# Kernel optimization log

Hardware: AMD Instinct MI355X
Metric: run time of the kernel (lower is better)

## Reference

```python
import jax, jax.numpy as jnp
import numpy as np

NUM_HIDDEN = 128
IN_DIM = 512  # num_hidden + num_in + num_vec*4 = 128 + 256 + 128
N_NODES = 50000
N_EDGES = 400000
BN_EPS = 1e-5


def setup_inputs() -> dict:
    key = jax.random.key(0)
    ks = jax.random.split(key, 12)
    h_V = jax.random.normal(ks[0], (N_NODES, NUM_HIDDEN), dtype=jnp.float32)
    h_E = jax.random.normal(ks[1], (N_EDGES, NUM_HIDDEN), dtype=jnp.float32)
    edge_idx = jax.random.randint(ks[2], (2, N_EDGES), 0, N_NODES, dtype=jnp.int64)
    batch_id = jnp.zeros((N_EDGES,), dtype=jnp.int32)
    vector_field_feat = jax.random.normal(ks[3], (N_EDGES, NUM_HIDDEN), dtype=jnp.float32)
    s = 1.0 / np.sqrt(IN_DIM)
    W11 = jax.random.uniform(ks[4], (IN_DIM, NUM_HIDDEN), jnp.float32, -s, s)
    b11 = jax.random.uniform(ks[5], (NUM_HIDDEN,), jnp.float32, -s, s)
    s2 = 1.0 / np.sqrt(NUM_HIDDEN)
    W12 = jax.random.uniform(ks[6], (NUM_HIDDEN, NUM_HIDDEN), jnp.float32, -s2, s2)
    b12 = jax.random.uniform(ks[7], (NUM_HIDDEN,), jnp.float32, -s2, s2)
    W13 = jax.random.uniform(ks[8], (NUM_HIDDEN, NUM_HIDDEN), jnp.float32, -s2, s2)
    b13 = jax.random.uniform(ks[9], (NUM_HIDDEN,), jnp.float32, -s2, s2)
    gamma = jnp.ones((NUM_HIDDEN,), dtype=jnp.float32)
    beta = jnp.zeros((NUM_HIDDEN,), dtype=jnp.float32)
    return {"h_V": h_V, "h_E": h_E, "edge_idx": edge_idx, "batch_id": batch_id,
            "vector_field_feat": vector_field_feat, "W11": W11, "b11": b11,
            "W12": W12, "b12": b12, "W13": W13, "b13": b13,
            "gamma": gamma, "beta": beta}


def reference(h_V, h_E, edge_idx, batch_id, vector_field_feat,
              W11, b11, W12, b12, W13, b13, gamma, beta):
    src_idx = edge_idx[0]
    dst_idx = edge_idx[1]
    # gather + concat: [E, 512]
    h_EV = jnp.concatenate([h_V[src_idx], h_E, h_V[dst_idx], vector_field_feat], axis=-1)
    # MLP: Linear-GELU-Linear-GELU-Linear (use_mlp_in_edge=True)
    h = jax.nn.gelu(h_EV @ W11 + b11, approximate=False)
    h = jax.nn.gelu(h @ W12 + b12, approximate=False)
    h_message = h @ W13 + b13
    # dropout is identity in eval; residual + BatchNorm1d over edge dim (batch stats)
    x = h_E + h_message
    mean = jnp.mean(x, axis=0)
    var = jnp.mean((x - mean) ** 2, axis=0)  # biased var, as BatchNorm uses
    out = (x - mean) * jax.lax.rsqrt(var + BN_EPS) * gamma + beta
    return out
```

## Files before the change

### kernel.cpp

```cpp
#include <hip/hip_runtime.h>
#include <hip/hip_bf16.h>
#include <math.h>

typedef __attribute__((ext_vector_type(8))) short  bf16x8;
typedef __attribute__((ext_vector_type(4))) float  f32x4;
typedef __attribute__((ext_vector_type(8))) unsigned short u16x8;

#define HID  128
#define BM   32
#define LROW 1024

__device__ __forceinline__ unsigned short f2bf(float f) {
    union { float f; unsigned u; } v; v.f = f;
    unsigned u = v.u;
    return (unsigned short)((u + 0x7fffu + ((u >> 16) & 1u)) >> 16);
}
__device__ __forceinline__ unsigned pkbf(float a, float b) {
    __hip_bfloat162 h2 = __float22bfloat162_rn(float2{a, b});
    union { __hip_bfloat162 h; unsigned u; } u; u.h = h2; return u.u;
}
__device__ __forceinline__ unsigned short bfr(float f) {
    __hip_bfloat16 h = __float2bfloat16(f);
    union { __hip_bfloat16 h; unsigned short s; } u; u.h = h; return u.s;
}
__device__ __forceinline__ float bf2f(unsigned short h) {
    union { unsigned u; float f; } v; v.u = ((unsigned)h) << 16;
    return v.f;
}
__device__ __forceinline__ float geluf(float x) {
    float x2 = x * x;
    float u  = __builtin_fmaf(0.044715f * x2, x, x);
    float e  = __builtin_amdgcn_exp2f(u * 2.30220795f);
    return x * e * __builtin_amdgcn_rcpf(e + 1.0f);
}

__global__ void prep_weights(const float* __restrict__ W11, const float* __restrict__ W12,
                             const float* __restrict__ W13,
                             unsigned short* __restrict__ wa, unsigned short* __restrict__ wc,
                             unsigned short* __restrict__ wbd,
                             unsigned short* __restrict__ w12t, unsigned short* __restrict__ w13t) {
    int idx = blockIdx.x * 256 + threadIdx.x;
    if (idx < 16384) {
        int k = idx >> 7, n = idx & 127;
        wa[n * 128 + k] = f2bf(W11[k * 128 + n]);
    } else if (idx < 32768) {
        int j = idx - 16384; int k = j >> 7, n = j & 127;
        wc[n * 128 + k] = f2bf(W11[(256 + k) * 128 + n]);
    } else if (idx < 65536) {
        int j = idx - 32768; int k = j >> 7, n = j & 127;
        int row = (k < 128) ? (128 + k) : (256 + k);
        wbd[n * 256 + k] = f2bf(W11[row * 128 + n]);
    } else if (idx < 81920) {
        int j = idx - 65536; int k = j >> 7, n = j & 127;
        w12t[n * 128 + k] = f2bf(W12[k * 128 + n]);
    } else if (idx < 98304) {
        int j = idx - 81920; int k = j >> 7, n = j & 127;
        w13t[n * 128 + k] = f2bf(W13[k * 128 + n]);
    }
}

__global__ __launch_bounds__(256, 4) void p_kernel(
    const float* __restrict__ hV,
    const unsigned short* __restrict__ wa, const unsigned short* __restrict__ wc,
    const float* __restrict__ b11,
    unsigned short* __restrict__ P1, unsigned short* __restrict__ P2, int nV)
{
    __shared__ __align__(16) char lds[BM * 512];
    const int tid = threadIdx.x, lane = tid & 63, wid = tid >> 6;
    const int lr = lane & 15, lh = lane >> 4;
    const int v0 = blockIdx.x * BM;

    {
        int r = tid >> 3, sub = tid & 7;
        int v = v0 + r; if (v >= nV) v = nV - 1;
        const float* sp = hV + (size_t)v * HID + sub * 16;
        f32x4 a0 = __builtin_nontemporal_load((const f32x4*)sp);
        f32x4 a1 = __builtin_nontemporal_load((const f32x4*)sp + 1);
        f32x4 a2 = __builtin_nontemporal_load((const f32x4*)sp + 2);
        f32x4 a3 = __builtin_nontemporal_load((const f32x4*)sp + 3);
        union { u16x8 s; unsigned u[4]; } pA, pB;
        pA.u[0] = pkbf(a0[0], a0[1]); pA.u[1] = pkbf(a0[2], a0[3]);
        pA.u[2] = pkbf(a1[0], a1[1]); pA.u[3] = pkbf(a1[2], a1[3]);
        pB.u[0] = pkbf(a2[0], a2[1]); pB.u[1] = pkbf(a2[2], a2[3]);
        pB.u[2] = pkbf(a3[0], a3[1]); pB.u[3] = pkbf(a3[2], a3[3]);
        int c0 = sub * 2, c1 = c0 + 1;
        int s0 = (c0 & 8) | ((c0 ^ r) & 7), s1 = (c1 & 8) | ((c1 ^ r) & 7);
        *(u16x8*)(lds + r * 512 + s0 * 16) = pA.s;
        *(u16x8*)(lds + r * 512 + s1 * 16) = pB.s;
    }
    __syncthreads();

    const int n0 = wid * 32 + lr, n1 = n0 + 16;
    f32x4 acc1[2][2], acc2[2][2];
#pragma unroll
    for (int j = 0; j < 2; ++j)
#pragma unroll
        for (int m = 0; m < 2; ++m) { acc1[j][m] = (f32x4){0,0,0,0}; acc2[j][m] = (f32x4){0,0,0,0}; }

    const unsigned short* a0p = wa + n0 * 128 + lh * 8;
    const unsigned short* a1p = wa + n1 * 128 + lh * 8;
    const unsigned short* c0p = wc + n0 * 128 + lh * 8;
    const unsigned short* c1p = wc + n1 * 128 + lh * 8;
#pragma unroll
    for (int kt = 0; kt < 4; ++kt) {
        bf16x8 ba0 = *(const bf16x8*)(a0p + kt * 32);
        bf16x8 ba1 = *(const bf16x8*)(a1p + kt * 32);
        bf16x8 bc0 = *(const bf16x8*)(c0p + kt * 32);
        bf16x8 bc1 = *(const bf16x8*)(c1p + kt * 32);
        int c = kt * 4 + lh;
#pragma unroll
        for (int m = 0; m < 2; ++m) {
            int row = m * 16 + lr;
            int sw  = (c & 8) | ((c ^ row) & 7);
            bf16x8 a = *(const bf16x8*)(lds + row * 512 + sw * 16);
            acc1[0][m] = __builtin_amdgcn_mfma_f32_16x16x32_bf16(a, ba0, acc1[0][m], 0, 0, 0);
            acc1[1][m] = __builtin_amdgcn_mfma_f32_16x16x32_bf16(a, ba1, acc1[1][m], 0, 0, 0);
            acc2[0][m] = __builtin_amdgcn_mfma_f32_16x16x32_bf16(a, bc0, acc2[0][m], 0, 0, 0);
            acc2[1][m] = __builtin_amdgcn_mfma_f32_16x16x32_bf16(a, bc1, acc2[1][m], 0, 0, 0);
        }
    }
    float bv0 = b11[n0], bv1 = b11[n1];
#pragma unroll
    for (int m = 0; m < 2; ++m)
#pragma unroll
        for (int i = 0; i < 4; ++i) {
            int row = m * 16 + lh * 4 + i;
            int v = v0 + row;
            if (v < nV) {
                size_t b = (size_t)v * HID;
                P1[b + n0] = bfr(acc1[0][m][i] + bv0);
                P1[b + n1] = bfr(acc1[1][m][i] + bv1);
                P2[b + n0] = bfr(acc2[0][m][i]);
                P2[b + n1] = bfr(acc2[1][m][i]);
            }
        }
}

template <int XBF16>
__global__ __launch_bounds__(256, 5) void edge_mlp_kernel(
    const float* __restrict__ hE, const int* __restrict__ eidx,
    const float* __restrict__ vff,
    const unsigned short* __restrict__ P1, const unsigned short* __restrict__ P2,
    const unsigned short* __restrict__ wbd, const unsigned short* __restrict__ w12t,
    const unsigned short* __restrict__ w13t,
    const float* __restrict__ b12, const float* __restrict__ b13,
    float* __restrict__ psum, float* __restrict__ psumsq,
    float* __restrict__ xf32, unsigned short* __restrict__ xbf16, int E)
{
    __shared__ __align__(16) char lds[BM * LROW];
    const int tid = threadIdx.x, lane = tid & 63, wid = tid >> 6;
    const int lr = lane & 15, lh = lane >> 4;
    const int e0 = blockIdx.x * BM;
    const bool idx64 = ((eidx[1] | eidx[3] | eidx[5] | eidx[7]) == 0);
    const int n0 = wid * 32 + lr, n1 = n0 + 16;

    {
        int r = tid >> 3, sub = tid & 7;
        int e = e0 + r;
        int sIdx = idx64 ? eidx[2 * e]       : eidx[e];
        int dIdx = idx64 ? eidx[2 * (E + e)] : eidx[E + e];
        int c0 = sub * 2, c1 = c0 + 1;
        int s0 = (c0 & 8) | ((c0 ^ r) & 7), s1 = (c1 & 8) | ((c1 ^ r) & 7);

        const float* spE = hE + (size_t)e * HID + sub * 16;
        f32x4 h0 = __builtin_nontemporal_load((const f32x4*)spE);
        f32x4 h1 = __builtin_nontemporal_load((const f32x4*)spE + 1);
        f32x4 h2 = __builtin_nontemporal_load((const f32x4*)spE + 2);
        f32x4 h3 = __builtin_nontemporal_load((const f32x4*)spE + 3);
        const unsigned short* p1p = P1 + (size_t)sIdx * HID + sub * 16;
        u16x8 g1a = *(const u16x8*)(p1p);
        u16x8 g1b = *(const u16x8*)(p1p + 8);
        {
            union { u16x8 s; unsigned u[4]; } cE0, cE1;
            cE0.u[0] = pkbf(h0[0], h0[1]); cE0.u[1] = pkbf(h0[2], h0[3]);
            cE0.u[2] = pkbf(h1[0], h1[1]); cE0.u[3] = pkbf(h1[2], h1[3]);
            cE1.u[0] = pkbf(h2[0], h2[1]); cE1.u[1] = pkbf(h2[2], h2[3]);
            cE1.u[2] = pkbf(h3[0], h3[1]); cE1.u[3] = pkbf(h3[2], h3[3]);
            *(u16x8*)(lds + r * LROW + 0 + s0 * 16) = cE0.s;
            *(u16x8*)(lds + r * LROW + 0 + s1 * 16) = cE1.s;
        }

        const float* spV = vff + (size_t)e * HID + sub * 16;
        f32x4 v0 = __builtin_nontemporal_load((const f32x4*)spV);
        f32x4 v1 = __builtin_nontemporal_load((const f32x4*)spV + 1);
        f32x4 v2 = __builtin_nontemporal_load((const f32x4*)spV + 2);
        f32x4 v3 = __builtin_nontemporal_load((const f32x4*)spV + 3);
        const unsigned short* p2p = P2 + (size_t)dIdx * HID + sub * 16;
        u16x8 g2a = *(const u16x8*)(p2p);
        u16x8 g2b = *(const u16x8*)(p2p + 8);
        {
            union { u16x8 s; unsigned u[4]; } cV0, cV1, pf0, pf1;
            cV0.u[0] = pkbf(v0[0], v0[1]); cV0.u[1] = pkbf(v0[2], v0[3]);
            cV0.u[2] = pkbf(v1[0], v1[1]); cV0.u[3] = pkbf(v1[2], v1[3]);
            cV1.u[0] = pkbf(v2[0], v2[1]); cV1.u[1] = pkbf(v2[2], v2[3]);
            cV1.u[2] = pkbf(v3[0], v3[1]); cV1.u[3] = pkbf(v3[2], v3[3]);
            *(u16x8*)(lds + r * LROW + 256 + s0 * 16) = cV0.s;
            *(u16x8*)(lds + r * LROW + 256 + s1 * 16) = cV1.s;
#pragma unroll
            for (int j = 0; j < 4; ++j) {
                pf0.u[j] = pkbf(bf2f(g1a[2 * j])     + bf2f(g2a[2 * j]),
                                bf2f(g1a[2 * j + 1]) + bf2f(g2a[2 * j + 1]));
                pf1.u[j] = pkbf(bf2f(g1b[2 * j])     + bf2f(g2b[2 * j]),
                                bf2f(g1b[2 * j + 1]) + bf2f(g2b[2 * j + 1]));
            }
            *(u16x8*)(lds + r * LROW + 768 + s0 * 16) = pf0.s;
            *(u16x8*)(lds + r * LROW + 768 + s1 * 16) = pf1.s;
        }
    }
    __syncthreads();

    f32x4 acc[2][2];
#pragma unroll
    for (int j = 0; j < 2; ++j)
#pragma unroll
        for (int m = 0; m < 2; ++m) acc[j][m] = (f32x4){0, 0, 0, 0};

    const unsigned short* w0p = wbd  + n0 * 256 + lh * 8;
    const unsigned short* w1p = wbd  + n1 * 256 + lh * 8;
    const unsigned short* q20 = w12t + n0 * 128 + lh * 8;
    const unsigned short* q21 = w12t + n1 * 128 + lh * 8;
    const unsigned short* q30 = w13t + n0 * 128 + lh * 8;
    const unsigned short* q31 = w13t + n1 * 128 + lh * 8;

    bf16x8 bA[4][2], bB[4][2];

#define PREF4(buf, p0, p1, base) \
    { _Pragma("unroll") for (int j = 0; j < 4; ++j) { \
        buf[j][0] = *(const bf16x8*)((p0) + ((base) + j) * 32); \
        buf[j][1] = *(const bf16x8*)((p1) + ((base) + j) * 32); } }

#define CONS4(buf, off) \
    { _Pragma("unroll") for (int j = 0; j < 4; ++j) { \
        int c = j * 4 + lh; \
        _Pragma("unroll") for (int m = 0; m < 2; ++m) { \
            int row = m * 16 + lr; \
            int sw  = (c & 8) | ((c ^ row) & 7); \
            bf16x8 a = *(const bf16x8*)(lds + row * LROW + (off) + sw * 16); \
            acc[0][m] = __builtin_amdgcn_mfma_f32_16x16x32_bf16(a, buf[j][0], acc[0][m], 0, 0, 0); \
            acc[1][m] = __builtin_amdgcn_mfma_f32_16x16x32_bf16(a, buf[j][1], acc[1][m], 0, 0, 0); } } }

    PREF4(bA, w0p, w1p, 0)
    PREF4(bB, w0p, w1p, 4)
    CONS4(bA, 0)
    CONS4(bB, 256)

    PREF4(bA, q20, q21, 0)

#pragma unroll
    for (int m = 0; m < 2; ++m)
#pragma unroll
        for (int i = 0; i < 4; ++i) {
            int row = m * 16 + lh * 4 + i;
            int ch0 = n0 >> 3, ch1 = n1 >> 3;
            int s0 = (ch0 & 8) | ((ch0 ^ row) & 7);
            int s1 = (ch1 & 8) | ((ch1 ^ row) & 7);
            float p0 = bf2f(*(const unsigned short*)(lds + row * LROW + 768 + s0 * 16 + (n0 & 7) * 2));
            float p1 = bf2f(*(const unsigned short*)(lds + row * LROW + 768 + s1 * 16 + (n1 & 7) * 2));
            float v0 = geluf(acc[0][m][i] + p0);
            float v1 = geluf(acc[1][m][i] + p1);
            *(unsigned short*)(lds + row * LROW + 512 + s0 * 16 + (n0 & 7) * 2) = bfr(v0);
            *(unsigned short*)(lds + row * LROW + 512 + s1 * 16 + (n1 & 7) * 2) = bfr(v1);
        }
    PREF4(bB, q30, q31, 0)
    __syncthreads();

#pragma unroll
    for (int j = 0; j < 2; ++j)
#pragma unroll
        for (int m = 0; m < 2; ++m) acc[j][m] = (f32x4){0, 0, 0, 0};
    CONS4(bA, 512)
    {
        float bv0 = b12[n0], bv1 = b12[n1];
#pragma unroll
        for (int m = 0; m < 2; ++m)
#pragma unroll
            for (int i = 0; i < 4; ++i) {
                int row = m * 16 + lh * 4 + i;
                int ch0 = n0 >> 3, ch1 = n1 >> 3;
                int s0 = (ch0 & 8) | ((ch0 ^ row) & 7);
                int s1 = (ch1 & 8) | ((ch1 ^ row) & 7);
                float v0 = geluf(acc[0][m][i] + bv0);
                float v1 = geluf(acc[1][m][i] + bv1);
                *(unsigned short*)(lds + row * LROW + 256 + s0 * 16 + (n0 & 7) * 2) = bfr(v0);
                *(unsigned short*)(lds + row * LROW + 256 + s1 * 16 + (n1 & 7) * 2) = bfr(v1);
            }
    }
    __syncthreads();

#pragma unroll
    for (int j = 0; j < 2; ++j)
#pragma unroll
        for (int m = 0; m < 2; ++m) acc[j][m] = (f32x4){0, 0, 0, 0};
    CONS4(bB, 256)

    {
        float bv0 = b13[n0], bv1 = b13[n1];
        float s0a = 0.f, q0a = 0.f, s1a = 0.f, q1a = 0.f;
#pragma unroll
        for (int m = 0; m < 2; ++m)
#pragma unroll
            for (int i = 0; i < 4; ++i) {
                int row = m * 16 + lh * 4 + i;
                int ch0 = n0 >> 3, ch1 = n1 >> 3;
                int s0 = (ch0 & 8) | ((ch0 ^ row) & 7);
                int s1 = (ch1 & 8) | ((ch1 ^ row) & 7);
                float he0 = bf2f(*(const unsigned short*)(lds + row * LROW + s0 * 16 + (n0 & 7) * 2));
                float he1 = bf2f(*(const unsigned short*)(lds + row * LROW + s1 * 16 + (n1 & 7) * 2));
                float x0 = acc[0][m][i] + bv0 + he0;
                float x1 = acc[1][m][i] + bv1 + he1;
                s0a += x0; q0a += x0 * x0;
                s1a += x1; q1a += x1 * x1;
                *(unsigned short*)(lds + row * LROW + 512 + s0 * 16 + (n0 & 7) * 2) = bfr(x0);
                *(unsigned short*)(lds + row * LROW + 512 + s1 * 16 + (n1 & 7) * 2) = bfr(x1);
            }
        s0a += __shfl_xor(s0a, 16); s0a += __shfl_xor(s0a, 32);
        q0a += __shfl_xor(q0a, 16); q0a += __shfl_xor(q0a, 32);
        s1a += __shfl_xor(s1a, 16); s1a += __shfl_xor(s1a, 32);
        q1a += __shfl_xor(q1a, 16); q1a += __shfl_xor(q1a, 32);
        if (lane < 16) {
            size_t base = (size_t)blockIdx.x * HID;
            psum[base + n0]   = s0a;
            psum[base + n1]   = s1a;
            psumsq[base + n0] = q0a;
            psumsq[base + n1] = q1a;
        }
    }
    __syncthreads();

    {
        int r = tid >> 3, sub = tid & 7;
        int c0 = sub * 2, c1 = c0 + 1;
        int s0 = (c0 & 8) | ((c0 ^ r) & 7), s1 = (c1 & 8) | ((c1 ^ r) & 7);
        u16x8 X0 = *(const u16x8*)(lds + r * LROW + 512 + s0 * 16);
        u16x8 X1 = *(const u16x8*)(lds + r * LROW + 512 + s1 * 16);
        size_t base = (size_t)(e0 + r) * HID;
        if (XBF16) {
            __builtin_nontemporal_store(X0, (u16x8*)(xbf16 + base + c0 * 8));
            __builtin_nontemporal_store(X1, (u16x8*)(xbf16 + base + c1 * 8));
        } else {
            f32x4 o0, o1, o2, o3;
#pragma unroll
            for (int e = 0; e < 4; ++e) {
                o0[e] = bf2f(X0[e]); o1[e] = bf2f(X0[4 + e]);
                o2[e] = bf2f(X1[e]); o3[e] = bf2f(X1[4 + e]);
            }
            __builtin_nontemporal_store(o0, (f32x4*)(xf32 + base + c0 * 8));
            __builtin_nontemporal_store(o1, (f32x4*)(xf32 + base + c0 * 8 + 4));
            __builtin_nontemporal_store(o2, (f32x4*)(xf32 + base + c1 * 8));
            __builtin_nontemporal_store(o3, (f32x4*)(xf32 + base + c1 * 8 + 4));
        }
    }
}

__global__ void bn_stats1(const float* __restrict__ psum, const float* __restrict__ psumsq,
                          float* __restrict__ part, int nblk) {
    int t = threadIdx.x;
    int c = t & 127, g = t >> 7;
    float s = 0.f, q = 0.f;
    for (int r = blockIdx.x * 2 + g; r < nblk; r += 128) {
        s += psum[(size_t)r * 128 + c];
        q += psumsq[(size_t)r * 128 + c];
    }
    __shared__ float ls[256], lq[256];
    ls[t] = s; lq[t] = q;
    __syncthreads();
    if (t < 128) {
        part[(size_t)blockIdx.x * 256 + c]       = ls[c] + ls[128 + c];
        part[(size_t)blockIdx.x * 256 + 128 + c] = lq[c] + lq[128 + c];
    }
}
__global__ void bn_stats2(const float* __restrict__ part,
                          const float* __restrict__ gamma, const float* __restrict__ beta,
                          float* __restrict__ params, float invE) {
    int c = threadIdx.x;
    if (c < 128) {
        float S = 0.f, Q = 0.f;
        for (int b = 0; b < 64; ++b) {
            S += part[(size_t)b * 256 + c];
            Q += part[(size_t)b * 256 + 128 + c];
        }
        float mean = S * invE;
        float var  = Q * invE - mean * mean;
        float sc   = gamma[c] * rsqrtf(var + 1e-5f);
        params[c]       = sc;
        params[128 + c] = beta[c] - mean * sc;
    }
}

__global__ void bn_apply_bf16(const unsigned short* __restrict__ x, float* __restrict__ out,
                              const float* __restrict__ params, int total8) {
    __shared__ float sc[128], sh[128];
    if (threadIdx.x < 128) { sc[threadIdx.x] = params[threadIdx.x]; sh[threadIdx.x] = params[128 + threadIdx.x]; }
    __syncthreads();
    int stride = gridDim.x * blockDim.x;
    for (int i = blockIdx.x * blockDim.x + threadIdx.x; i < total8; i += stride) {
        size_t base = (size_t)i * 8;
        u16x8 v = __builtin_nontemporal_load((const u16x8*)(x + base));
        int c0 = (int)(base & 127);
        f32x4 o0, o1;
#pragma unroll
        for (int e = 0; e < 4; ++e) o0[e] = bf2f(v[e]) * sc[c0 + e] + sh[c0 + e];
#pragma unroll
        for (int e = 0; e < 4; ++e) o1[e] = bf2f(v[4 + e]) * sc[c0 + 4 + e] + sh[c0 + 4 + e];
        __builtin_nontemporal_store(o0, (f32x4*)(out + base));
        __builtin_nontemporal_store(o1, (f32x4*)(out + base + 4));
    }
}

__global__ void bn_apply_f32(float* __restrict__ x, const float* __restrict__ params, int total4) {
    __shared__ float sc[128], sh[128];
    if (threadIdx.x < 128) { sc[threadIdx.x] = params[threadIdx.x]; sh[threadIdx.x] = params[128 + threadIdx.x]; }
    __syncthreads();
    int stride = gridDim.x * blockDim.x;
    for (int i = blockIdx.x * blockDim.x + threadIdx.x; i < total4; i += stride) {
        size_t base = (size_t)i * 4;
        f32x4 v = *(f32x4*)(x + base);
        int c0 = (int)(base & 127);
#pragma unroll
        for (int e = 0; e < 4; ++e) v[e] = v[e] * sc[c0 + e] + sh[c0 + e];
        *(f32x4*)(x + base) = v;
    }
}

extern "C" void kernel_launch(void* const* d_in, const int* in_sizes, int n_in,
                              void* d_out, int out_size, void* d_ws, size_t ws_size,
                              hipStream_t stream) {
    const float* hV    = (const float*)d_in[0];
    const float* hE    = (const float*)d_in[1];
    const int*   eidx  = (const int*)d_in[2];
    const float* vff   = (const float*)d_in[4];
    const float* W11   = (const float*)d_in[5];
    const float* b11   = (const float*)d_in[6];
    const float* W12   = (const float*)d_in[7];
    const float* b12   = (const float*)d_in[8];
    const float* W13   = (const float*)d_in[9];
    const float* b13   = (const float*)d_in[10];
    const float* gamma = (const float*)d_in[11];
    const float* beta  = (const float*)d_in[12];

    const int nV    = in_sizes[0] / HID;
    const int E     = in_sizes[1] / HID;
    const int nblk  = E / BM;
    const int nblkV = (nV + BM - 1) / BM;
    const int nVp   = nblkV * BM;

    float* params = (float*)d_ws;
    float* part   = params + 256;
    unsigned short* wa   = (unsigned short*)(part + 64 * 256);
    unsigned short* wc   = wa   + 16384;
    unsigned short* wbd  = wc   + 16384;
    unsigned short* w12t = wbd  + 32768;
    unsigned short* w13t = w12t + 16384;
    float* psum   = (float*)(w13t + 16384);
    float* psumsq = psum + (size_t)nblk * HID;
    unsigned short* P1 = (unsigned short*)(psumsq + (size_t)nblk * HID);
    unsigned short* P2 = P1 + (size_t)nVp * HID;
    unsigned short* xbf = P2 + (size_t)nVp * HID;
    const size_t fixed = (size_t)((char*)xbf - (char*)d_ws);
    const bool useBf = ws_size >= fixed + (size_t)E * HID * 2;

    prep_weights<<<384, 256, 0, stream>>>(W11, W12, W13, wa, wc, wbd, w12t, w13t);
    p_kernel<<<nblkV, 256, 0, stream>>>(hV, wa, wc, b11, P1, P2, nV);

    if (useBf)
        edge_mlp_kernel<1><<<nblk, 256, 0, stream>>>(hE, eidx, vff, P1, P2, wbd, w12t, w13t,
                                                     b12, b13, psum, psumsq,
                                                     (float*)d_out, xbf, E);
    else
        edge_mlp_kernel<0><<<nblk, 256, 0, stream>>>(hE, eidx, vff, P1, P2, wbd, w12t, w13t,
                                                     b12, b13, psum, psumsq,
                                                     (float*)d_out, xbf, E);

    bn_stats1<<<64, 256, 0, stream>>>(psum, psumsq, part, nblk);
    bn_stats2<<<1, 128, 0, stream>>>(part, gamma, beta, params, 1.0f / (float)E);

    if (useBf)
        bn_apply_bf16<<<2048, 256, 0, stream>>>(xbf, (float*)d_out, params, E * HID / 8);
    else
        bn_apply_f32<<<2048, 256, 0, stream>>>((float*)d_out, params, E * HID / 4);
}
```

Measured before the change: 445.3 us.

## Process two edge tiles per block and prefetch second tile during first's MLP

Each edge-MLP block now handles two 32-edge tiles instead of one. The second tile's index, h_E/vff loads and P1/P2 gathers are issued while the first tile's GEMM and GELU stages run, so global-memory latency is hidden behind MFMA work. Batch-norm partial sums are accumulated across both tiles, which halves the number of partial rows. The occupancy hint drops from 5 to 4 blocks per CU to make room for the extra registers, and P1/P2 now live in the output buffer when the bf16 path is taken, which shrinks the workspace that path needs.

```diff
diff --git a/kernel.cpp b/kernel.cpp
--- a/kernel.cpp
+++ b/kernel.cpp
@@ -137,7 +137,7 @@
 }
 
 template <int XBF16>
-__global__ __launch_bounds__(256, 5) void edge_mlp_kernel(
+__global__ __launch_bounds__(256, 4) void edge_mlp_kernel(
     const float* __restrict__ hE, const int* __restrict__ eidx,
     const float* __restrict__ vff,
     const unsigned short* __restrict__ P1, const unsigned short* __restrict__ P2,
@@ -150,70 +150,23 @@
     __shared__ __align__(16) char lds[BM * LROW];
     const int tid = threadIdx.x, lane = tid & 63, wid = tid >> 6;
     const int lr = lane & 15, lh = lane >> 4;
-    const int e0 = blockIdx.x * BM;
+    const int e0 = blockIdx.x * (2 * BM);
     const bool idx64 = ((eidx[1] | eidx[3] | eidx[5] | eidx[7]) == 0);
     const int n0 = wid * 32 + lr, n1 = n0 + 16;
 
-    {
-        int r = tid >> 3, sub = tid & 7;
-        int e = e0 + r;
-        int sIdx = idx64 ? eidx[2 * e]       : eidx[e];
-        int dIdx = idx64 ? eidx[2 * (E + e)] : eidx[E + e];
-        int c0 = sub * 2, c1 = c0 + 1;
-        int s0 = (c0 & 8) | ((c0 ^ r) & 7), s1 = (c1 & 8) | ((c1 ^ r) & 7);
-
-        const float* spE = hE + (size_t)e * HID + sub * 16;
-        f32x4 h0 = __builtin_nontemporal_load((const f32x4*)spE);
-        f32x4 h1 = __builtin_nontemporal_load((const f32x4*)spE + 1);
-        f32x4 h2 = __builtin_nontemporal_load((const f32x4*)spE + 2);
-        f32x4 h3 = __builtin_nontemporal_load((const f32x4*)spE + 3);
-        const unsigned short* p1p = P1 + (size_t)sIdx * HID + sub * 16;
-        u16x8 g1a = *(const u16x8*)(p1p);
-        u16x8 g1b = *(const u16x8*)(p1p + 8);
-        {
-            union { u16x8 s; unsigned u[4]; } cE0, cE1;
-            cE0.u[0] = pkbf(h0[0], h0[1]); cE0.u[1] = pkbf(h0[2], h0[3]);
-            cE0.u[2] = pkbf(h1[0], h1[1]); cE0.u[3] = pkbf(h1[2], h1[3]);
-            cE1.u[0] = pkbf(h2[0], h2[1]); cE1.u[1] = pkbf(h2[2], h2[3]);
-            cE1.u[2] = pkbf(h3[0], h3[1]); cE1.u[3] = pkbf(h3[2], h3[3]);
-            *(u16x8*)(lds + r * LROW + 0 + s0 * 16) = cE0.s;
-            *(u16x8*)(lds + r * LROW + 0 + s1 * 16) = cE1.s;
-        }
-
-        const float* spV = vff + (size_t)e * HID + sub * 16;
-        f32x4 v0 = __builtin_nontemporal_load((const f32x4*)spV);
-        f32x4 v1 = __builtin_nontemporal_load((const f32x4*)spV + 1);
-        f32x4 v2 = __builtin_nontemporal_load((const f32x4*)spV + 2);
-        f32x4 v3 = __builtin_nontemporal_load((const f32x4*)spV + 3);
-        const unsigned short* p2p = P2 + (size_t)dIdx * HID + sub * 16;
-        u16x8 g2a = *(const u16x8*)(p2p);
-        u16x8 g2b = *(const u16x8*)(p2p + 8);
-        {
-            union { u16x8 s; unsigned u[4]; } cV0, cV1, pf0, pf1;
-            cV0.u[0] = pkbf(v0[0], v0[1]); cV0.u[1] = pkbf(v0[2], v0[3]);
-            cV0.u[2] = pkbf(v1[0], v1[1]); cV0.u[3] = pkbf(v1[2], v1[3]);
-            cV1.u[0] = pkbf(v2[0], v2[1]); cV1.u[1] = pkbf(v2[2], v2[3]);
-            cV1.u[2] = pkbf(v3[0], v3[1]); cV1.u[3] = pkbf(v3[2], v3[3]);
-            *(u16x8*)(lds + r * LROW + 256 + s0 * 16) = cV0.s;
-            *(u16x8*)(lds + r * LROW + 256 + s1 * 16) = cV1.s;
-#pragma unroll
-            for (int j = 0; j < 4; ++j) {
-                pf0.u[j] = pkbf(bf2f(g1a[2 * j])     + bf2f(g2a[2 * j]),
-                                bf2f(g1a[2 * j + 1]) + bf2f(g2a[2 * j + 1]));
-                pf1.u[j] = pkbf(bf2f(g1b[2 * j])     + bf2f(g2b[2 * j]),
-                                bf2f(g1b[2 * j + 1]) + bf2f(g2b[2 * j + 1]));
-            }
-            *(u16x8*)(lds + r * LROW + 768 + s0 * 16) = pf0.s;
-            *(u16x8*)(lds + r * LROW + 768 + s1 * 16) = pf1.s;
-        }
-    }
-    __syncthreads();
-
+    const int r = tid >> 3, sub = tid & 7;
+    const int sc0 = sub * 2, sc1 = sc0 + 1;
+    const int sl0 = (sc0 & 8) | ((sc0 ^ r) & 7), sl1 = (sc1 & 8) | ((sc1 ^ r) & 7);
+
+    const float bv12_0 = b12[n0], bv12_1 = b12[n1];
+    const float bv13_0 = b13[n0], bv13_1 = b13[n1];
+
+    f32x4 A0, A1, A2, A3, B0, B1, B2, B3;
+    u16x8 G1A, G1B, G2A, G2B;
+    int sIdx, dIdx;
+    float s0a = 0.f, q0a = 0.f, s1a = 0.f, q1a = 0.f;
     f32x4 acc[2][2];
-#pragma unroll
-    for (int j = 0; j < 2; ++j)
-#pragma unroll
-        for (int m = 0; m < 2; ++m) acc[j][m] = (f32x4){0, 0, 0, 0};
+    bf16x8 bA[4][2], bB[4][2];
 
     const unsigned short* w0p = wbd  + n0 * 256 + lh * 8;
     const unsigned short* w1p = wbd  + n1 * 256 + lh * 8;
@@ -222,7 +175,46 @@
     const unsigned short* q30 = w13t + n0 * 128 + lh * 8;
     const unsigned short* q31 = w13t + n1 * 128 + lh * 8;
 
-    bf16x8 bA[4][2], bB[4][2];
+#define STAGE_EIDX(E0T) { int e = (E0T) + r; \
+    sIdx = idx64 ? eidx[2 * e]       : eidx[e]; \
+    dIdx = idx64 ? eidx[2 * (E + e)] : eidx[E + e]; }
+
+#define ISSUE_EV(E0T) { int e = (E0T) + r; \
+    const f32x4* pE = (const f32x4*)(hE  + (size_t)e * HID + sub * 16); \
+    const f32x4* pV = (const f32x4*)(vff + (size_t)e * HID + sub * 16); \
+    A0 = __builtin_nontemporal_load(pE + 0); A1 = __builtin_nontemporal_load(pE + 1); \
+    A2 = __builtin_nontemporal_load(pE + 2); A3 = __builtin_nontemporal_load(pE + 3); \
+    B0 = __builtin_nontemporal_load(pV + 0); B1 = __builtin_nontemporal_load(pV + 1); \
+    B2 = __builtin_nontemporal_load(pV + 2); B3 = __builtin_nontemporal_load(pV + 3); }
+
+#define ISSUE_P() { \
+    const u16x8* p1 = (const u16x8*)(P1 + (size_t)sIdx * HID + sub * 16); \
+    const u16x8* p2 = (const u16x8*)(P2 + (size_t)dIdx * HID + sub * 16); \
+    G1A = p1[0]; G1B = p1[1]; G2A = p2[0]; G2B = p2[1]; }
+
+#define WRITE_EV() { union { u16x8 s; unsigned u[4]; } cE0, cE1, cV0, cV1; \
+    cE0.u[0] = pkbf(A0[0], A0[1]); cE0.u[1] = pkbf(A0[2], A0[3]); \
+    cE0.u[2] = pkbf(A1[0], A1[1]); cE0.u[3] = pkbf(A1[2], A1[3]); \
+    cE1.u[0] = pkbf(A2[0], A2[1]); cE1.u[1] = pkbf(A2[2], A2[3]); \
+    cE1.u[2] = pkbf(A3[0], A3[1]); cE1.u[3] = pkbf(A3[2], A3[3]); \
+    cV0.u[0] = pkbf(B0[0], B0[1]); cV0.u[1] = pkbf(B0[2], B0[3]); \
+    cV0.u[2] = pkbf(B1[0], B1[1]); cV0.u[3] = pkbf(B1[2], B1[3]); \
+    cV1.u[0] = pkbf(B2[0], B2[1]); cV1.u[1] = pkbf(B2[2], B2[3]); \
+    cV1.u[2] = pkbf(B3[0], B3[1]); cV1.u[3] = pkbf(B3[2], B3[3]); \
+    *(u16x8*)(lds + r * LROW +   0 + sl0 * 16) = cE0.s; \
+    *(u16x8*)(lds + r * LROW +   0 + sl1 * 16) = cE1.s; \
+    *(u16x8*)(lds + r * LROW + 256 + sl0 * 16) = cV0.s; \
+    *(u16x8*)(lds + r * LROW + 256 + sl1 * 16) = cV1.s; }
+
+#define WRITE_P() { union { u16x8 s; unsigned u[4]; } pf0, pf1; \
+    _Pragma("unroll") for (int j = 0; j < 4; ++j) { \
+        pf0.u[j] = pkbf(bf2f(G1A[2*j]) + bf2f(G2A[2*j]), bf2f(G1A[2*j+1]) + bf2f(G2A[2*j+1])); \
+        pf1.u[j] = pkbf(bf2f(G1B[2*j]) + bf2f(G2B[2*j]), bf2f(G1B[2*j+1]) + bf2f(G2B[2*j+1])); } \
+    *(u16x8*)(lds + r * LROW + 768 + sl0 * 16) = pf0.s; \
+    *(u16x8*)(lds + r * LROW + 768 + sl1 * 16) = pf1.s; }
+
+#define ACCZERO { _Pragma("unroll") for (int j = 0; j < 2; ++j) \
+    _Pragma("unroll") for (int m = 0; m < 2; ++m) acc[j][m] = (f32x4){0, 0, 0, 0}; }
 
 #define PREF4(buf, p0, p1, base) \
     { _Pragma("unroll") for (int j = 0; j < 4; ++j) { \
@@ -239,116 +231,116 @@
             acc[0][m] = __builtin_amdgcn_mfma_f32_16x16x32_bf16(a, buf[j][0], acc[0][m], 0, 0, 0); \
             acc[1][m] = __builtin_amdgcn_mfma_f32_16x16x32_bf16(a, buf[j][1], acc[1][m], 0, 0, 0); } } }
 
+#define GELU1_PHASE() { _Pragma("unroll") for (int m = 0; m < 2; ++m) \
+    _Pragma("unroll") for (int i = 0; i < 4; ++i) { \
+        int row = m * 16 + lh * 4 + i; int ch0 = n0 >> 3, ch1 = n1 >> 3; \
+        int t0 = (ch0 & 8) | ((ch0 ^ row) & 7), t1 = (ch1 & 8) | ((ch1 ^ row) & 7); \
+        float p0 = bf2f(*(const unsigned short*)(lds + row * LROW + 768 + t0 * 16 + (n0 & 7) * 2)); \
+        float p1 = bf2f(*(const unsigned short*)(lds + row * LROW + 768 + t1 * 16 + (n1 & 7) * 2)); \
+        float v0 = geluf(acc[0][m][i] + p0), v1 = geluf(acc[1][m][i] + p1); \
+        *(unsigned short*)(lds + row * LROW + 512 + t0 * 16 + (n0 & 7) * 2) = bfr(v0); \
+        *(unsigned short*)(lds + row * LROW + 512 + t1 * 16 + (n1 & 7) * 2) = bfr(v1); } }
+
+#define GELU2_PHASE() { _Pragma("unroll") for (int m = 0; m < 2; ++m) \
+    _Pragma("unroll") for (int i = 0; i < 4; ++i) { \
+        int row = m * 16 + lh * 4 + i; int ch0 = n0 >> 3, ch1 = n1 >> 3; \
+        int t0 = (ch0 & 8) | ((ch0 ^ row) & 7), t1 = (ch1 & 8) | ((ch1 ^ row) & 7); \
+        float v0 = geluf(acc[0][m][i] + bv12_0), v1 = geluf(acc[1][m][i] + bv12_1); \
+        *(unsigned short*)(lds + row * LROW + 256 + t0 * 16 + (n0 & 7) * 2) = bfr(v0); \
+        *(unsigned short*)(lds + row * LROW + 256 + t1 * 16 + (n1 & 7) * 2) = bfr(v1); } }
+
+#define EPILOGUE_PHASE() { _Pragma("unroll") for (int m = 0; m < 2; ++m) \
+    _Pragma("unroll") for (int i = 0; i < 4; ++i) { \
+        int row = m * 16 + lh * 4 + i; int ch0 = n0 >> 3, ch1 = n1 >> 3; \
+        int t0 = (ch0 & 8) | ((ch0 ^ row) & 7), t1 = (ch1 & 8) | ((ch1 ^ row) & 7); \
+        float he0 = bf2f(*(const unsigned short*)(lds + row * LROW + t0 * 16 + (n0 & 7) * 2)); \
+        float he1 = bf2f(*(const unsigned short*)(lds + row * LROW + t1 * 16 + (n1 & 7) * 2)); \
+        float x0 = acc[0][m][i] + bv13_0 + he0; \
+        float x1 = acc[1][m][i] + bv13_1 + he1; \
+        s0a += x0; q0a += x0 * x0; s1a += x1; q1a += x1 * x1; \
+        *(unsigned short*)(lds + row * LROW + 512 + t0 * 16 + (n0 & 7) * 2) = bfr(x0); \
+        *(unsigned short*)(lds + row * LROW + 512 + t1 * 16 + (n1 & 7) * 2) = bfr(x1); } }
+
+#define XWRITE_PHASE(E0T) { \
+    u16x8 X0 = *(const u16x8*)(lds + r * LROW + 512 + sl0 * 16); \
+    u16x8 X1 = *(const u16x8*)(lds + r * LROW + 512 + sl1 * 16); \
+    size_t base = (size_t)((E0T) + r) * HID; \
+    if (XBF16) { \
+        __builtin_nontemporal_store(X0, (u16x8*)(xbf16 + base + sc0 * 8)); \
+        __builtin_nontemporal_store(X1, (u16x8*)(xbf16 + base + sc1 * 8)); \
+    } else { \
+        f32x4 o0, o1, o2, o3; \
+        _Pragma("unroll") for (int e = 0; e < 4; ++e) { \
+            o0[e] = bf2f(X0[e]); o1[e] = bf2f(X0[4 + e]); \
+            o2[e] = bf2f(X1[e]); o3[e] = bf2f(X1[4 + e]); } \
+        __builtin_nontemporal_store(o0, (f32x4*)(xf32 + base + sc0 * 8)); \
+        __builtin_nontemporal_store(o1, (f32x4*)(xf32 + base + sc0 * 8 + 4)); \
+        __builtin_nontemporal_store(o2, (f32x4*)(xf32 + base + sc1 * 8)); \
+        __builtin_nontemporal_store(o3, (f32x4*)(xf32 + base + sc1 * 8 + 4)); } }
+
+    STAGE_EIDX(e0); ISSUE_EV(e0); ISSUE_P();
+    WRITE_EV(); WRITE_P();
+    __syncthreads();
+
+    ACCZERO;
     PREF4(bA, w0p, w1p, 0)
     PREF4(bB, w0p, w1p, 4)
     CONS4(bA, 0)
     CONS4(bB, 256)
-
     PREF4(bA, q20, q21, 0)
-
-#pragma unroll
-    for (int m = 0; m < 2; ++m)
-#pragma unroll
-        for (int i = 0; i < 4; ++i) {
-            int row = m * 16 + lh * 4 + i;
-            int ch0 = n0 >> 3, ch1 = n1 >> 3;
-            int s0 = (ch0 & 8) | ((ch0 ^ row) & 7);
-            int s1 = (ch1 & 8) | ((ch1 ^ row) & 7);
-            float p0 = bf2f(*(const unsigned short*)(lds + row * LROW + 768 + s0 * 16 + (n0 & 7) * 2));
-            float p1 = bf2f(*(const unsigned short*)(lds + row * LROW + 768 + s1 * 16 + (n1 & 7) * 2));
-            float v0 = geluf(acc[0][m][i] + p0);
-            float v1 = geluf(acc[1][m][i] + p1);
-            *(unsigned short*)(lds + row * LROW + 512 + s0 * 16 + (n0 & 7) * 2) = bfr(v0);
-            *(unsigned short*)(lds + row * LROW + 512 + s1 * 16 + (n1 & 7) * 2) = bfr(v1);
-        }
+    GELU1_PHASE()
     PREF4(bB, q30, q31, 0)
     __syncthreads();
 
-#pragma unroll
-    for (int j = 0; j < 2; ++j)
-#pragma unroll
-        for (int m = 0; m < 2; ++m) acc[j][m] = (f32x4){0, 0, 0, 0};
+    ACCZERO;
     CONS4(bA, 512)
-    {
-        float bv0 = b12[n0], bv1 = b12[n1];
-#pragma unroll
-        for (int m = 0; m < 2; ++m)
-#pragma unroll
-            for (int i = 0; i < 4; ++i) {
-                int row = m * 16 + lh * 4 + i;
-                int ch0 = n0 >> 3, ch1 = n1 >> 3;
-                int s0 = (ch0 & 8) | ((ch0 ^ row) & 7);
-                int s1 = (ch1 & 8) | ((ch1 ^ row) & 7);
-                float v0 = geluf(acc[0][m][i] + bv0);
-                float v1 = geluf(acc[1][m][i] + bv1);
-                *(unsigned short*)(lds + row * LROW + 256 + s0 * 16 + (n0 & 7) * 2) = bfr(v0);
-                *(unsigned short*)(lds + row * LROW + 256 + s1 * 16 + (n1 & 7) * 2) = bfr(v1);
-            }
-    }
-    __syncthreads();
-
-#pragma unroll
-    for (int j = 0; j < 2; ++j)
-#pragma unroll
-        for (int m = 0; m < 2; ++m) acc[j][m] = (f32x4){0, 0, 0, 0};
+    GELU2_PHASE()
+    STAGE_EIDX(e0 + BM); ISSUE_EV(e0 + BM);
+    __syncthreads();
+
+    ACCZERO;
     CONS4(bB, 256)
-
-    {
-        float bv0 = b13[n0], bv1 = b13[n1];
-        float s0a = 0.f, q0a = 0.f, s1a = 0.f, q1a = 0.f;
-#pragma unroll
-        for (int m = 0; m < 2; ++m)
-#pragma unroll
-            for (int i = 0; i < 4; ++i) {
-                int row = m * 16 + lh * 4 + i;
-                int ch0 = n0 >> 3, ch1 = n1 >> 3;
-                int s0 = (ch0 & 8) | ((ch0 ^ row) & 7);
-                int s1 = (ch1 & 8) | ((ch1 ^ row) & 7);
-                float he0 = bf2f(*(const unsigned short*)(lds + row * LROW + s0 * 16 + (n0 & 7) * 2));
-                float he1 = bf2f(*(const unsigned short*)(lds + row * LROW + s1 * 16 + (n1 & 7) * 2));
-                float x0 = acc[0][m][i] + bv0 + he0;
-                float x1 = acc[1][m][i] + bv1 + he1;
-                s0a += x0; q0a += x0 * x0;
-                s1a += x1; q1a += x1 * x1;
-                *(unsigned short*)(lds + row * LROW + 512 + s0 * 16 + (n0 & 7) * 2) = bfr(x0);
-                *(unsigned short*)(lds + row * LROW + 512 + s1 * 16 + (n1 & 7) * 2) = bfr(x1);
-            }
-        s0a += __shfl_xor(s0a, 16); s0a += __shfl_xor(s0a, 32);
-        q0a += __shfl_xor(q0a, 16); q0a += __shfl_xor(q0a, 32);
-        s1a += __shfl_xor(s1a, 16); s1a += __shfl_xor(s1a, 32);
-        q1a += __shfl_xor(q1a, 16); q1a += __shfl_xor(q1a, 32);
-        if (lane < 16) {
-            size_t base = (size_t)blockIdx.x * HID;
-            psum[base + n0]   = s0a;
-            psum[base + n1]   = s1a;
-            psumsq[base + n0] = q0a;
-            psumsq[base + n1] = q1a;
-        }
-    }
-    __syncthreads();
-
-    {
-        int r = tid >> 3, sub = tid & 7;
-        int c0 = sub * 2, c1 = c0 + 1;
-        int s0 = (c0 & 8) | ((c0 ^ r) & 7), s1 = (c1 & 8) | ((c1 ^ r) & 7);
-        u16x8 X0 = *(const u16x8*)(lds + r * LROW + 512 + s0 * 16);
-        u16x8 X1 = *(const u16x8*)(lds + r * LROW + 512 + s1 * 16);
-        size_t base = (size_t)(e0 + r) * HID;
-        if (XBF16) {
-            __builtin_nontemporal_store(X0, (u16x8*)(xbf16 + base + c0 * 8));
-            __builtin_nontemporal_store(X1, (u16x8*)(xbf16 + base + c1 * 8));
-        } else {
-            f32x4 o0, o1, o2, o3;
-#pragma unroll
-            for (int e = 0; e < 4; ++e) {
-                o0[e] = bf2f(X0[e]); o1[e] = bf2f(X0[4 + e]);
-                o2[e] = bf2f(X1[e]); o3[e] = bf2f(X1[4 + e]);
-            }
-            __builtin_nontemporal_store(o0, (f32x4*)(xf32 + base + c0 * 8));
-            __builtin_nontemporal_store(o1, (f32x4*)(xf32 + base + c0 * 8 + 4));
-            __builtin_nontemporal_store(o2, (f32x4*)(xf32 + base + c1 * 8));
-            __builtin_nontemporal_store(o3, (f32x4*)(xf32 + base + c1 * 8 + 4));
-        }
+    ISSUE_P();
+    EPILOGUE_PHASE()
+    WRITE_P();
+    __syncthreads();
+
+    XWRITE_PHASE(e0)
+    WRITE_EV()
+    PREF4(bA, w0p, w1p, 0)
+    PREF4(bB, w0p, w1p, 4)
+    __syncthreads();
+
+    ACCZERO;
+    CONS4(bA, 0)
+    CONS4(bB, 256)
+    PREF4(bA, q20, q21, 0)
+    GELU1_PHASE()
+    PREF4(bB, q30, q31, 0)
+    __syncthreads();
+
+    ACCZERO;
+    CONS4(bA, 512)
+    GELU2_PHASE()
+    __syncthreads();
+
+    ACCZERO;
+    CONS4(bB, 256)
+    EPILOGUE_PHASE()
+    __syncthreads();
+
+    XWRITE_PHASE(e0 + BM)
+
+    s0a += __shfl_xor(s0a, 16); s0a += __shfl_xor(s0a, 32);
+    q0a += __shfl_xor(q0a, 16); q0a += __shfl_xor(q0a, 32);
+    s1a += __shfl_xor(s1a, 16); s1a += __shfl_xor(s1a, 32);
+    q1a += __shfl_xor(q1a, 16); q1a += __shfl_xor(q1a, 32);
+    if (lane < 16) {
+        size_t base = (size_t)blockIdx.x * HID;
+        psum[base + n0]   = s0a;
+        psum[base + n1]   = s1a;
+        psumsq[base + n0] = q0a;
+        psumsq[base + n1] = q1a;
     }
 }
 
@@ -440,7 +432,7 @@
 
     const int nV    = in_sizes[0] / HID;
     const int E     = in_sizes[1] / HID;
-    const int nblk  = E / BM;
+    const int nblk  = E / (2 * BM);
     const int nblkV = (nV + BM - 1) / BM;
     const int nVp   = nblkV * BM;
 
@@ -453,11 +445,19 @@
     unsigned short* w13t = w12t + 16384;
     float* psum   = (float*)(w13t + 16384);
     float* psumsq = psum + (size_t)nblk * HID;
-    unsigned short* P1 = (unsigned short*)(psumsq + (size_t)nblk * HID);
-    unsigned short* P2 = P1 + (size_t)nVp * HID;
-    unsigned short* xbf = P2 + (size_t)nVp * HID;
-    const size_t fixed = (size_t)((char*)xbf - (char*)d_ws);
-    const bool useBf = ws_size >= fixed + (size_t)E * HID * 2;
+    char*  after  = (char*)(psumsq + (size_t)nblk * HID);
+    size_t off    = ((size_t)(after - (char*)d_ws) + 15) & ~(size_t)15;
+
+    const bool useBf = ws_size >= off + (size_t)E * HID * 2;
+    unsigned short *P1, *P2, *xbf = nullptr;
+    if (useBf) {
+        P1  = (unsigned short*)d_out;
+        P2  = P1 + (size_t)nVp * HID;
+        xbf = (unsigned short*)((char*)d_ws + off);
+    } else {
+        P1  = (unsigned short*)((char*)d_ws + off);
+        P2  = P1 + (size_t)nVp * HID;
+    }
 
     prep_weights<<<384, 256, 0, stream>>>(W11, W12, W13, wa, wc, wbd, w12t, w13t);
     p_kernel<<<nblkV, 256, 0, stream>>>(hV, wa, wc, b11, P1, P2, nV);
```

Result: faster. 423.9 us (-4.8%).

## Shrink edge LDS rows, prefetch layer-2 weights earlier, reuse output buffer for P

Applied to the files above, without the earlier changes.

The edge kernel's LDS row stride drops from 1024 to 768 bytes: the layer-1 GELU output is now written in place over the precomputed P1+P2 slot instead of into a separate region. Separate register buffers for the W12 and W13 fragments let the W12 prefetch start during the first GEMM, at the cost of more registers; the launch-bounds occupancy hint drops from 5 to 4 to allow that. On the host, P1/P2 now live in the output buffer when the bf16 path is taken, so the workspace only has to hold the bf16 x array. This relies on the edge kernel not writing d_out in bf16 mode.

```diff
diff --git a/kernel.cpp b/kernel.cpp
--- a/kernel.cpp
+++ b/kernel.cpp
@@ -8,7 +8,7 @@
 
 #define HID  128
 #define BM   32
-#define LROW 1024
+#define LROW 768
 
 __device__ __forceinline__ unsigned short f2bf(float f) {
     union { float f; unsigned u; } v; v.f = f;
@@ -137,7 +137,7 @@
 }
 
 template <int XBF16>
-__global__ __launch_bounds__(256, 5) void edge_mlp_kernel(
+__global__ __launch_bounds__(256, 4) void edge_mlp_kernel(
     const float* __restrict__ hE, const int* __restrict__ eidx,
     const float* __restrict__ vff,
     const unsigned short* __restrict__ P1, const unsigned short* __restrict__ P2,
@@ -203,8 +203,8 @@
                 pf1.u[j] = pkbf(bf2f(g1b[2 * j])     + bf2f(g2b[2 * j]),
                                 bf2f(g1b[2 * j + 1]) + bf2f(g2b[2 * j + 1]));
             }
-            *(u16x8*)(lds + r * LROW + 768 + s0 * 16) = pf0.s;
-            *(u16x8*)(lds + r * LROW + 768 + s1 * 16) = pf1.s;
+            *(u16x8*)(lds + r * LROW + 512 + s0 * 16) = pf0.s;
+            *(u16x8*)(lds + r * LROW + 512 + s1 * 16) = pf1.s;
         }
     }
     __syncthreads();
@@ -222,7 +222,7 @@
     const unsigned short* q30 = w13t + n0 * 128 + lh * 8;
     const unsigned short* q31 = w13t + n1 * 128 + lh * 8;
 
-    bf16x8 bA[4][2], bB[4][2];
+    bf16x8 bA[4][2], bB[4][2], b2[4][2], b3[4][2];
 
 #define PREF4(buf, p0, p1, base) \
     { _Pragma("unroll") for (int j = 0; j < 4; ++j) { \
@@ -242,9 +242,8 @@
     PREF4(bA, w0p, w1p, 0)
     PREF4(bB, w0p, w1p, 4)
     CONS4(bA, 0)
+    PREF4(b2, q20, q21, 0)
     CONS4(bB, 256)
-
-    PREF4(bA, q20, q21, 0)
 
 #pragma unroll
     for (int m = 0; m < 2; ++m)
@@ -254,21 +253,23 @@
             int ch0 = n0 >> 3, ch1 = n1 >> 3;
             int s0 = (ch0 & 8) | ((ch0 ^ row) & 7);
             int s1 = (ch1 & 8) | ((ch1 ^ row) & 7);
-            float p0 = bf2f(*(const unsigned short*)(lds + row * LROW + 768 + s0 * 16 + (n0 & 7) * 2));
-            float p1 = bf2f(*(const unsigned short*)(lds + row * LROW + 768 + s1 * 16 + (n1 & 7) * 2));
+            char* a0 = lds + row * LROW + 512 + s0 * 16 + (n0 & 7) * 2;
+            char* a1 = lds + row * LROW + 512 + s1 * 16 + (n1 & 7) * 2;
+            float p0 = bf2f(*(const unsigned short*)a0);
+            float p1 = bf2f(*(const unsigned short*)a1);
             float v0 = geluf(acc[0][m][i] + p0);
             float v1 = geluf(acc[1][m][i] + p1);
-            *(unsigned short*)(lds + row * LROW + 512 + s0 * 16 + (n0 & 7) * 2) = bfr(v0);
-            *(unsigned short*)(lds + row * LROW + 512 + s1 * 16 + (n1 & 7) * 2) = bfr(v1);
-        }
-    PREF4(bB, q30, q31, 0)
+            *(unsigned short*)a0 = bfr(v0);
+            *(unsigned short*)a1 = bfr(v1);
+        }
+    PREF4(b3, q30, q31, 0)
     __syncthreads();
 
 #pragma unroll
     for (int j = 0; j < 2; ++j)
 #pragma unroll
         for (int m = 0; m < 2; ++m) acc[j][m] = (f32x4){0, 0, 0, 0};
-    CONS4(bA, 512)
+    CONS4(b2, 512)
     {
         float bv0 = b12[n0], bv1 = b12[n1];
 #pragma unroll
@@ -291,7 +292,7 @@
     for (int j = 0; j < 2; ++j)
 #pragma unroll
         for (int m = 0; m < 2; ++m) acc[j][m] = (f32x4){0, 0, 0, 0};
-    CONS4(bB, 256)
+    CONS4(b3, 256)
 
     {
         float bv0 = b13[n0], bv1 = b13[n1];
@@ -453,11 +454,19 @@
     unsigned short* w13t = w12t + 16384;
     float* psum   = (float*)(w13t + 16384);
     float* psumsq = psum + (size_t)nblk * HID;
-    unsigned short* P1 = (unsigned short*)(psumsq + (size_t)nblk * HID);
-    unsigned short* P2 = P1 + (size_t)nVp * HID;
-    unsigned short* xbf = P2 + (size_t)nVp * HID;
-    const size_t fixed = (size_t)((char*)xbf - (char*)d_ws);
-    const bool useBf = ws_size >= fixed + (size_t)E * HID * 2;
+    char*  after  = (char*)(psumsq + (size_t)nblk * HID);
+    size_t off    = ((size_t)(after - (char*)d_ws) + 15) & ~(size_t)15;
+
+    const bool useBf = ws_size >= off + (size_t)E * HID * 2;
+    unsigned short *P1, *P2, *xbf = nullptr;
+    if (useBf) {
+        P1  = (unsigned short*)d_out;
+        P2  = P1 + (size_t)nVp * HID;
+        xbf = (unsigned short*)((char*)d_ws + off);
+    } else {
+        P1  = (unsigned short*)((char*)d_ws + off);
+        P2  = P1 + (size_t)nVp * HID;
+    }
 
     prep_weights<<<384, 256, 0, stream>>>(W11, W12, W13, wa, wc, wbd, w12t, w13t);
     p_kernel<<<nblkV, 256, 0, stream>>>(hV, wa, wc, b11, P1, P2, nV);
```

Result: faster. 426.9 us (-4.1%).
